# Kernel tuning notes

Measured on AMD Instinct MI355X. Metric: run time of the kernel, lower is better.

The kernel has to match this reference:

```python
import jax, jax.numpy as jnp
import numpy as np

UP = 2
CUTOFF = 1.0 / UP  # factor = 1


def make_recon_rect(N, cutoff):
    """Reconstruction low-pass rect for rfft2, shape [N, N//2+1]."""
    lo = int(N * cutoff // 2)
    hi = int(N - lo)
    r = np.ones(N, dtype=np.float32)
    r[lo + 1:hi] = 0.0
    if N % 4 == 0:
        r[lo] = 0.5
        r[hi] = 0.5
    rect2d = r[:, None] * r[None, :]          # [N, N]
    return jnp.asarray(rect2d[:, :N // 2 + 1])  # keep rfft half-spectrum


def setup_inputs() -> dict:
    key = jax.random.key(0)
    x = jax.random.normal(key, (16, 64, 128, 128), dtype=jnp.float32)
    return {"x": x}


def reference(x):
    B, C, H, W = x.shape
    Hu, Wu = H * UP, W * UP
    # zero-insertion upsample: sample at (i*UP, j*UP), zeros elsewhere
    z = jnp.zeros((B, C, Hu, Wu), dtype=x.dtype).at[:, :, ::UP, ::UP].set(x)
    rect = make_recon_rect(Wu, CUTOFF)         # [Wu, Wu//2+1]
    xf = jnp.fft.rfft2(z) * rect               # low-pass in frequency domain
    out = jnp.fft.irfft2(xf) * (UP ** 2)       # gain correction
    return out
```

## Files before the change

kernel.cpp:

```cpp
#include <hip/hip_runtime.h>


typedef __bf16 bf16x8 __attribute__((ext_vector_type(8)));
typedef float  f32x4  __attribute__((ext_vector_type(4)));

#define PI_D 3.14159265358979323846

constexpr double csin(double x) {
    double t = x, s = x; const double x2 = x * x;
    for (int k = 1; k < 13; ++k) { t *= -x2 / double((2 * k) * (2 * k + 1)); s += t; }
    return s;
}
constexpr double ccos(double x) {
    double t = 1.0, s = 1.0; const double x2 = x * x;
    for (int k = 1; k < 13; ++k) { t *= -x2 / double((2 * k - 1) * (2 * k)); s += t; }
    return s;
}
constexpr unsigned short d2bf(double v) {
    unsigned short sgn = 0;
    if (v < 0) { sgn = 0x8000; v = -v; }
    if (v == 0) return sgn;
    int e = 0;
    while (v >= 2.0) { v *= 0.5; ++e; }
    while (v < 1.0)  { v *= 2.0; --e; }
    double m = (v - 1.0) * 128.0;
    int mi = (int)m;
    const double frac = m - (double)mi;
    if (frac > 0.5 || (frac == 0.5 && (mi & 1))) ++mi;
    if (mi == 128) { mi = 0; ++e; }
    return (unsigned short)(sgn | ((unsigned)(e + 127) << 7) | (unsigned)mi);
}
constexpr double gval(int j) {
    const int d = 2 * (j & 127) + 1;
    const double th = PI_D * (double)d / 256.0;
    const double s = ((d & 3) == 1) ? 1.0 : -1.0;
    return s * ccos(th) / (128.0 * csin(th));
}
struct GhTab { unsigned short v[8 * 64 * 8]; };
constexpr GhTab make_ghtab() {
    GhTab t{};
    for (int dd = 0; dd < 8; ++dd)
        for (int lane = 0; lane < 64; ++lane) {
            const int l15 = lane & 15, l4 = lane >> 4;
            const int base = l15 - 8 * l4 + 16 * dd;
            for (int e = 0; e < 8; ++e)
                t.v[(dd * 64 + lane) * 8 + e] = d2bf(gval(base - e));
        }
    return t;
}
__device__ constexpr GhTab GHTAB = make_ghtab();

__device__ __forceinline__ unsigned short f2bf(float x) {
    unsigned int b = __float_as_uint(x);
    return (unsigned short)((b + 0x7FFFu + ((b >> 16) & 1u)) >> 16);
}

__device__ __forceinline__ int etswz(int row) {
    return (((row & 7) ^ (((row >> 3) & 3) << 1) ^ (((row >> 5) & 1) << 2)) << 4);
}

__global__ __launch_bounds__(512, 4)
void upsample_fused(const float* __restrict__ xin, float* __restrict__ out)
{
    __shared__ __align__(16) unsigned short Et[64 * 128];

    const unsigned short* __restrict__ ghtab = GHTAB.v;

    const int tid  = threadIdx.x;
    const int lane = tid & 63;
    const int w    = tid >> 6;
    const int l15  = lane & 15;
    const int l4   = lane >> 4;

    const long long img = blockIdx.x >> 2;
    const int qb        = blockIdx.x & 3;
    const float* __restrict__ xim = xin + img * (128LL * 128LL);
    float*       __restrict__ oim = out + img * (256LL * 256LL);

    const int r = 16 * w + l15;
    const float* __restrict__ xrow = xim + r * 128;

    float4 xlo[4], xhi[4];
    #pragma unroll
    for (int t = 0; t < 4; ++t) {
        xlo[t] = *(const float4*)&xrow[32 * t + 8 * l4];
        xhi[t] = *(const float4*)&xrow[32 * t + 8 * l4 + 4];
    }

    bf16x8 ghc[8];
    #pragma unroll
    for (int v = 0; v < 8; ++v) {
        const int dd = (v + 2 * qb) & 7;
        ghc[v] = *(const bf16x8*)&ghtab[(dd * 64 + lane) * 8];
    }

    bf16x8 xa[4];
    #pragma unroll
    for (int t = 0; t < 4; ++t) {
        union { bf16x8 v; unsigned short u[8]; } H;
        H.u[0] = f2bf(xlo[t].x); H.u[1] = f2bf(xlo[t].y);
        H.u[2] = f2bf(xlo[t].z); H.u[3] = f2bf(xlo[t].w);
        H.u[4] = f2bf(xhi[t].x); H.u[5] = f2bf(xhi[t].y);
        H.u[6] = f2bf(xhi[t].z); H.u[7] = f2bf(xhi[t].w);
        xa[t] = H.v;
        if (t == qb) {
            #pragma unroll
            for (int e = 0; e < 8; ++e) {
                const int row = 16 * l4 + 2 * e;
                Et[row * 128 + (((2 * r) ^ etswz(row)) >> 1)] = H.u[e];
            }
        }
    }

    float* __restrict__ orow = oim + (2 * r) * 256;
    #pragma unroll
    for (int j = 0; j < 2; ++j) {
        f32x4 acc = {0.f, 0.f, 0.f, 0.f};
        #pragma unroll
        for (int t = 0; t < 4; ++t)
            acc = __builtin_amdgcn_mfma_f32_16x16x32_bf16(ghc[(j - 2 * t) & 7],
                                                          xa[t], acc, 0, 0, 0);
        const int i0g = 32 * qb + 16 * j + 4 * l4;
        float4 xc = *(const float4*)&xrow[i0g];
        float4 o0 = make_float4(xc.x, acc[0], xc.y, acc[1]);
        float4 o1 = make_float4(xc.z, acc[2], xc.w, acc[3]);
        *(float4*)&orow[2 * i0g]     = o0;
        *(float4*)&orow[2 * i0g + 4] = o1;
        #pragma unroll
        for (int q = 0; q < 4; ++q) {
            const int row = 2 * (16 * j + 4 * l4 + q) + 1;
            Et[row * 128 + (((2 * r) ^ etswz(row)) >> 1)] = f2bf(acc[q]);
        }
    }
    __syncthreads();

    {
        const int pa = w & 3;
        const int mh = w >> 2;
        bf16x8 gbd[4];
        #pragma unroll
        for (int d = 0; d < 4; ++d) {
            const int dd = (pa + 2 * d) & 7;
            gbd[d] = *(const bf16x8*)&ghtab[(dd * 64 + lane) * 8];
        }
        float* __restrict__ prowA = oim + (2 * (16 * pa + l15) + 1) * 256 + 64 * qb;
        float* __restrict__ prowB = oim + (2 * (16 * (pa + 4) + l15) + 1) * 256 + 64 * qb;
        #pragma unroll
        for (int mci = 0; mci < 2; ++mci) {
            const int mc = 2 * mh + mci;
            const int row = 16 * mc + l15;
            const char* erow = (const char*)Et + row * 256;
            const int sw = etswz(row);
            f32x4 aA = {0.f, 0.f, 0.f, 0.f};
            f32x4 aB = {0.f, 0.f, 0.f, 0.f};
            #pragma unroll
            for (int t = 0; t < 4; ++t) {
                bf16x8 ef = *(const bf16x8*)(erow + ((64 * t + 16 * l4) ^ sw));
                aA = __builtin_amdgcn_mfma_f32_16x16x32_bf16(ef, gbd[(-t) & 3], aA, 0, 0, 0);
                aB = __builtin_amdgcn_mfma_f32_16x16x32_bf16(ef, gbd[(2 - t) & 3], aB, 0, 0, 0);
            }
            float4 oA = make_float4(aA[0], aA[1], aA[2], aA[3]);
            float4 oB = make_float4(aB[0], aB[1], aB[2], aB[3]);
            *(float4*)&prowA[16 * mc + 4 * l4] = oA;
            *(float4*)&prowB[16 * mc + 4 * l4] = oB;
        }
    }
}

extern "C" void kernel_launch(void* const* d_in, const int* in_sizes, int n_in,
                              void* d_out, int out_size, void* d_ws, size_t ws_size,
                              hipStream_t stream)
{
    (void)n_in; (void)out_size; (void)d_ws; (void)ws_size;
    const float* x = (const float*)d_in[0];
    float* out = (float*)d_out;
    int nimg = in_sizes[0] / (128 * 128);

    hipLaunchKernelGGL(upsample_fused, dim3(nimg * 4), dim3(512), 0, stream, x, out);
}
```

Before: 91.05 us.

## Process two images per block with prefetch of next image's input rows

Each block now handles two consecutive images in sequence. The next image's input rows are loaded into registers while the current image's MFMA work runs, and a separate LDS buffer is used per image so the second phase does not need a barrier before writing. The full __syncthreads is replaced by an lgkmcnt wait plus a raw s_barrier. The grid is halved, and LDS per block doubles, which may lower occupancy. An odd image count would leave the last image unprocessed.

New measurement: 132.7 us. 1.46x slower.

```diff
diff --git a/kernel.cpp b/kernel.cpp
--- a/kernel.cpp
+++ b/kernel.cpp
@@ -59,41 +59,16 @@
     return (((row & 7) ^ (((row >> 3) & 3) << 1) ^ (((row >> 5) & 1) << 2)) << 4);
 }
 
-__global__ __launch_bounds__(512, 4)
-void upsample_fused(const float* __restrict__ xin, float* __restrict__ out)
+__device__ __forceinline__ void tile_phase(
+    const unsigned short* __restrict__ ghtab,
+    const float* __restrict__ xrow,
+    const float* __restrict__ nxrow,
+    float* __restrict__ oim,
+    unsigned short* __restrict__ Et,
+    float4 (&xlo)[4], float4 (&xhi)[4],
+    const int qb, const int lane, const int w,
+    const int l15, const int l4, const int r)
 {
-    __shared__ __align__(16) unsigned short Et[64 * 128];
-
-    const unsigned short* __restrict__ ghtab = GHTAB.v;
-
-    const int tid  = threadIdx.x;
-    const int lane = tid & 63;
-    const int w    = tid >> 6;
-    const int l15  = lane & 15;
-    const int l4   = lane >> 4;
-
-    const long long img = blockIdx.x >> 2;
-    const int qb        = blockIdx.x & 3;
-    const float* __restrict__ xim = xin + img * (128LL * 128LL);
-    float*       __restrict__ oim = out + img * (256LL * 256LL);
-
-    const int r = 16 * w + l15;
-    const float* __restrict__ xrow = xim + r * 128;
-
-    float4 xlo[4], xhi[4];
-    #pragma unroll
-    for (int t = 0; t < 4; ++t) {
-        xlo[t] = *(const float4*)&xrow[32 * t + 8 * l4];
-        xhi[t] = *(const float4*)&xrow[32 * t + 8 * l4 + 4];
-    }
-
-    bf16x8 ghc[8];
-    #pragma unroll
-    for (int v = 0; v < 8; ++v) {
-        const int dd = (v + 2 * qb) & 7;
-        ghc[v] = *(const bf16x8*)&ghtab[(dd * 64 + lane) * 8];
-    }
-
     bf16x8 xa[4];
     #pragma unroll
     for (int t = 0; t < 4; ++t) {
@@ -112,6 +87,21 @@
         }
     }
 
+    if (nxrow) {
+        #pragma unroll
+        for (int t = 0; t < 4; ++t) {
+            xlo[t] = *(const float4*)&nxrow[32 * t + 8 * l4];
+            xhi[t] = *(const float4*)&nxrow[32 * t + 8 * l4 + 4];
+        }
+    }
+
+    bf16x8 ghc[8];
+    #pragma unroll
+    for (int v = 0; v < 8; ++v) {
+        const int dd = (v + 2 * qb) & 7;
+        ghc[v] = *(const bf16x8*)&ghtab[(dd * 64 + lane) * 8];
+    }
+
     float* __restrict__ orow = oim + (2 * r) * 256;
     #pragma unroll
     for (int j = 0; j < 2; ++j) {
@@ -132,7 +122,10 @@
             Et[row * 128 + (((2 * r) ^ etswz(row)) >> 1)] = f2bf(acc[q]);
         }
     }
-    __syncthreads();
+
+    asm volatile("s_waitcnt lgkmcnt(0)" ::: "memory");
+    __builtin_amdgcn_s_barrier();
+    __builtin_amdgcn_sched_barrier(0);
 
     {
         const int pa = w & 3;
@@ -167,6 +160,44 @@
     }
 }
 
+__global__ __launch_bounds__(512, 4)
+void upsample_fused(const float* __restrict__ xin, float* __restrict__ out)
+{
+    __shared__ __align__(16) unsigned short Et0[64 * 128];
+    __shared__ __align__(16) unsigned short Et1[64 * 128];
+
+    const unsigned short* __restrict__ ghtab = GHTAB.v;
+
+    const int tid  = threadIdx.x;
+    const int lane = tid & 63;
+    const int w    = tid >> 6;
+    const int l15  = lane & 15;
+    const int l4   = lane >> 4;
+
+    const int bid = blockIdx.x;
+    const int qb  = bid & 3;
+    const long long img0 = (long long)(bid >> 2) * 2;
+
+    const float* __restrict__ xim0 = xin + img0 * (128LL * 128LL);
+    const float* __restrict__ xim1 = xim0 + 128LL * 128LL;
+    float* __restrict__ oim0 = out + img0 * (256LL * 256LL);
+    float* __restrict__ oim1 = oim0 + 256LL * 256LL;
+
+    const int r = 16 * w + l15;
+    const float* __restrict__ xrow0 = xim0 + r * 128;
+    const float* __restrict__ xrow1 = xim1 + r * 128;
+
+    float4 xlo[4], xhi[4];
+    #pragma unroll
+    for (int t = 0; t < 4; ++t) {
+        xlo[t] = *(const float4*)&xrow0[32 * t + 8 * l4];
+        xhi[t] = *(const float4*)&xrow0[32 * t + 8 * l4 + 4];
+    }
+
+    tile_phase(ghtab, xrow0, xrow1, oim0, Et0, xlo, xhi, qb, lane, w, l15, l4, r);
+    tile_phase(ghtab, xrow1, nullptr, oim1, Et1, xlo, xhi, qb, lane, w, l15, l4, r);
+}
+
 extern "C" void kernel_launch(void* const* d_in, const int* in_sizes, int n_in,
                               void* d_out, int out_size, void* d_ws, size_t ws_size,
                               hipStream_t stream)
@@ -175,6 +206,7 @@
     const float* x = (const float*)d_in[0];
     float* out = (float*)d_out;
     int nimg = in_sizes[0] / (128 * 128);
-
-    hipLaunchKernelGGL(upsample_fused, dim3(nimg * 4), dim3(512), 0, stream, x, out);
-}
+    int nblk = (nimg >> 1) * 4;
+
+    hipLaunchKernelGGL(upsample_fused, dim3(nblk), dim3(512), 0, stream, x, out);
+}
```
